# Kernel optimization log

Measured on AMD Instinct MI355X. Metric: run time of the kernel, lower is better.

The kernel has to match this reference:

```python
import jax, jax.numpy as jnp
import numpy as np

B, L, D_MODEL = 2, 4096, 256
D_STATE, D_CONV, EXPAND = 16, 4, 2
D_INNER = EXPAND * D_MODEL
DT_RANK = D_MODEL // 16
D_FF = 2048


def setup_inputs() -> dict:
    key = jax.random.key(0)
    ks = jax.random.split(key, 14)
    s = 0.02
    A_log = jnp.log(jnp.tile(jnp.arange(1, D_STATE + 1, dtype=jnp.float32), (D_INNER, 1)))
    return {
        "x": jax.random.normal(ks[0], (B, L, D_MODEL), jnp.float32),
        "in_proj_w": jax.random.normal(ks[1], (2 * D_INNER, D_MODEL), jnp.float32) * s,
        "conv_w": jax.random.normal(ks[2], (D_INNER, D_CONV), jnp.float32) * s,
        "conv_b": jax.random.normal(ks[3], (D_INNER,), jnp.float32) * s,
        "x_proj_w": jax.random.normal(ks[4], (DT_RANK + 2 * D_STATE, D_INNER), jnp.float32) * s,
        "dt_proj_w": jax.random.normal(ks[5], (D_INNER, DT_RANK), jnp.float32) * s,
        "dt_proj_b": jax.random.uniform(ks[6], (D_INNER,), jnp.float32, -4.0, -2.0),
        "A_log": A_log,
        "D": jnp.ones((D_INNER,), jnp.float32),
        "out_proj_w": jax.random.normal(ks[7], (D_MODEL, D_INNER), jnp.float32) * s,
        "lin1_w": jax.random.normal(ks[8], (D_FF, D_MODEL), jnp.float32) * s,
        "lin1_b": jnp.zeros((D_FF,), jnp.float32),
        "lin2_w": jax.random.normal(ks[9], (D_FF, D_FF), jnp.float32) * s,
        "lin2_b": jnp.zeros((D_FF,), jnp.float32),
    }


def reference(x, in_proj_w, conv_w, conv_b, x_proj_w, dt_proj_w, dt_proj_b,
              A_log, D, out_proj_w, lin1_w, lin1_b, lin2_w, lin2_b):
    b, l, _ = x.shape
    d_inner = conv_w.shape[0]
    d_state = A_log.shape[1]
    dt_rank = dt_proj_w.shape[1]
    d_conv = conv_w.shape[1]

    # in_proj -> split into x and gate z
    xz = x @ in_proj_w.T                       # (B,L,2*Din)
    xin, z = jnp.split(xz, 2, axis=-1)

    # causal depthwise conv1d + SiLU
    xc = jnp.transpose(xin, (0, 2, 1))         # (B,Din,L)
    xc = jax.lax.conv_general_dilated(
        xc, conv_w[:, None, :], (1,), [(d_conv - 1, 0)],
        dimension_numbers=("NCH", "OIH", "NCH"), feature_group_count=d_inner)
    xc = xc + conv_b[None, :, None]
    u = jax.nn.silu(jnp.transpose(xc, (0, 2, 1)))  # (B,L,Din)

    # input-dependent SSM params
    x_dbl = u @ x_proj_w.T                     # (B,L,dt_rank+2*N)
    dt, Bt, Ct = jnp.split(x_dbl, [dt_rank, dt_rank + d_state], axis=-1)
    delta = jax.nn.softplus(dt @ dt_proj_w.T + dt_proj_b)  # (B,L,Din)

    A = -jnp.exp(A_log)                        # (Din,N)
    dA = jnp.exp(delta[..., None] * A)         # (B,L,Din,N)
    dBu = delta[..., None] * Bt[:, :, None, :] * u[..., None]  # (B,L,Din,N)

    def step(h, inp):
        dA_t, dBu_t, C_t = inp
        h = dA_t * h + dBu_t                   # (B,Din,N)
        y = jnp.einsum("bdn,bn->bd", h, C_t)
        return h, y

    h0 = jnp.zeros((b, d_inner, d_state), x.dtype)
    _, ys = jax.lax.scan(step, h0, (jnp.swapaxes(dA, 0, 1),
                                    jnp.swapaxes(dBu, 0, 1),
                                    jnp.swapaxes(Ct, 0, 1)))
    y = jnp.swapaxes(ys, 0, 1) + u * D         # (B,L,Din)
    y = y * jax.nn.silu(z)
    m = y @ out_proj_w.T                       # (B,L,d_model)

    # trailing MLP: lin2(relu(lin1(.)))
    h1 = jax.nn.relu(m @ lin1_w.T + lin1_b)
    return h1 @ lin2_w.T + lin2_b
```

## Files before the change

### kernel.cpp

```cpp
#include <hip/hip_runtime.h>
#include <hip/hip_bf16.h>
#include <stdint.h>

#define BB  2
#define LL  4096
#define DM  256
#define DI  512
#define NST 16
#define DTR 16
#define DFF 2048
#define ML  (BB*LL)

#define NCHUNK 128
#define CHUNK  32
#define BDN    (BB*DI*NST)

typedef __attribute__((ext_vector_type(8))) short s16x8;
typedef __attribute__((ext_vector_type(4))) float f32x4;

__device__ __forceinline__ ushort f2bf(float f) {
  union { float f; uint32_t u; } v; v.f = f;
  return (ushort)((v.u + 0x7FFFu + ((v.u >> 16) & 1u)) >> 16);
}

__device__ __forceinline__ void async16(const void* g, void* l) {
  __builtin_amdgcn_global_load_lds(
      (const __attribute__((address_space(1))) void*)g,
      (__attribute__((address_space(3))) void*)l, 16, 0, 0);
}

__global__ void k_f2b(const float* __restrict__ src, ushort* __restrict__ dst, int n4) {
  int i = blockIdx.x * 256 + threadIdx.x;
  if (i >= n4) return;
  f32x4 v = ((const f32x4*)src)[i];
  *(ushort4*)&dst[i * 4] = make_ushort4(f2bf(v[0]), f2bf(v[1]), f2bf(v[2]), f2bf(v[3]));
}

__global__ void k_xprojw(const float* __restrict__ src, ushort* __restrict__ dst) {
  int i = blockIdx.x * 256 + threadIdx.x;
  if (i >= 128 * DI / 4) return;
  int e = i * 4;
  int r = e >> 9;
  int c = e & 511;
  ushort4 o;
  if (r < DTR + 2 * NST) {
    f32x4 v = *(const f32x4*)&src[r * DI + c];
    o = make_ushort4(f2bf(v[0]), f2bf(v[1]), f2bf(v[2]), f2bf(v[3]));
  } else {
    o = make_ushort4(0, 0, 0, 0);
  }
  *(ushort4*)&dst[e] = o;
}

template<int OUTF, int OUTB, int BIAS, int RELU>
__global__ __launch_bounds__(256)
void k_gemm(const ushort* __restrict__ A, const ushort* __restrict__ W,
            const float* __restrict__ bias,
            float* __restrict__ outF, ushort* __restrict__ outB,
            int M, int N, int K) {
  __shared__ __align__(16) ushort AsB[3][128 * 32];
  __shared__ __align__(16) ushort BsB[3][128 * 32];
  const int tid  = threadIdx.x;
  const int lane = tid & 63;
  const int wv   = tid >> 6;

  const int nwg  = gridDim.x * gridDim.y;
  const int flat = blockIdx.y * gridDim.x + blockIdx.x;
  const int cpx  = nwg >> 3;
  const int swz  = (nwg & 7) ? flat : (flat & 7) * cpx + (flat >> 3);
  const int m0 = (swz / gridDim.x) << 7;
  const int n0 = (swz % gridDim.x) << 7;

  const int wr = (wv >> 1) << 6;
  const int wc = (wv & 1) << 6;
  const int lr = lane & 15;
  const int hi = lane >> 4;

  f32x4 acc[4][4] = {};

  const int sr0 = (wv << 5) + (lane >> 2);
  const int sc  = lane & 3;
  const int nt = K >> 5;

  auto STAGE = [&](int t, int bi) {
    const int k0 = t << 5;
#pragma unroll
    for (int j = 0; j < 2; ++j) {
      const int r  = sr0 + j * 16;
      const int cs = sc ^ ((r >> 1) & 3);
      async16(A + (size_t)(m0 + r) * K + k0 + cs * 8, &AsB[bi][((wv << 5) + j * 16) * 32]);
      async16(W + (size_t)(n0 + r) * K + k0 + cs * 8, &BsB[bi][((wv << 5) + j * 16) * 32]);
    }
  };

  STAGE(0, 0);
  STAGE(1, 1);

  int cur = 0;
  for (int t = 0; t < nt; ++t) {
    if (t + 1 < nt) { asm volatile("s_waitcnt vmcnt(4)" ::: "memory"); }
    else            { asm volatile("s_waitcnt vmcnt(0)" ::: "memory"); }
    __builtin_amdgcn_s_barrier();
    __builtin_amdgcn_sched_barrier(0);

    if (t + 2 < nt) {
      int nx2 = cur + 2; if (nx2 >= 3) nx2 -= 3;
      STAGE(t + 2, nx2);
    }

    const ushort* As = AsB[cur];
    const ushort* Bs = BsB[cur];
    s16x8 af[4], bf_[4];
#pragma unroll
    for (int mi = 0; mi < 4; ++mi) {
      const int row = wr + mi * 16 + lr;
      af[mi] = *(const s16x8*)&As[row * 32 + ((hi ^ ((row >> 1) & 3)) << 3)];
    }
#pragma unroll
    for (int ni = 0; ni < 4; ++ni) {
      const int row = wc + ni * 16 + lr;
      bf_[ni] = *(const s16x8*)&Bs[row * 32 + ((hi ^ ((row >> 1) & 3)) << 3)];
    }
    asm volatile("s_waitcnt lgkmcnt(0)" ::: "memory");
    __builtin_amdgcn_sched_barrier(0);

    __builtin_amdgcn_s_setprio(1);
#pragma unroll
    for (int mi = 0; mi < 4; ++mi)
#pragma unroll
      for (int ni = 0; ni < 4; ++ni)
        acc[mi][ni] = __builtin_amdgcn_mfma_f32_16x16x32_bf16(af[mi], bf_[ni], acc[mi][ni], 0, 0, 0);
    __builtin_amdgcn_s_setprio(0);

    cur = (cur + 1 == 3) ? 0 : cur + 1;
  }

#pragma unroll
  for (int mi = 0; mi < 4; ++mi) {
#pragma unroll
    for (int ni = 0; ni < 4; ++ni) {
      const int gc = n0 + wc + ni * 16 + lr;
      const float b = BIAS ? bias[gc] : 0.f;
#pragma unroll
      for (int i = 0; i < 4; ++i) {
        const int gr = m0 + wr + mi * 16 + (hi << 2) + i;
        float v = acc[mi][ni][i] + b;
        if (RELU) v = fmaxf(v, 0.f);
        if (OUTF) outF[(size_t)gr * N + gc] = v;
        if (OUTB) outB[(size_t)gr * N + gc] = f2bf(v);
      }
    }
  }
}

template<int OUTF, int OUTB, int BIAS, int RELU>
__global__ __launch_bounds__(512, 2)
void k_gemm256(const ushort* __restrict__ A, const ushort* __restrict__ W,
               const float* __restrict__ bias,
               float* __restrict__ outF, ushort* __restrict__ outB,
               int M, int N, int K) {
  __shared__ __align__(16) ushort AsB[4][256 * 32];
  __shared__ __align__(16) ushort BsB[4][256 * 32];
  const int tid  = threadIdx.x;
  const int lane = tid & 63;
  const int wv   = tid >> 6;

  const int nwg  = gridDim.x * gridDim.y;
  const int flat = blockIdx.y * gridDim.x + blockIdx.x;
  const int cpx  = nwg >> 3;
  const int swz  = (nwg & 7) ? flat : (flat & 7) * cpx + (flat >> 3);
  const int m0 = (swz / gridDim.x) << 8;
  const int n0 = (swz % gridDim.x) << 8;

  const int wrM = (wv >> 2) << 7;
  const int wcN = (wv & 3) << 6;
  const int lr = lane & 15;
  const int hi = lane >> 4;

  f32x4 acc[8][4] = {};

  const int sr0 = (wv << 5) + (lane >> 2);
  const int sc  = lane & 3;
  const int nt  = K >> 5;

  auto STAGE = [&](int t, int bi) {
    const int k0 = t << 5;
#pragma unroll
    for (int j = 0; j < 2; ++j) {
      const int r  = sr0 + j * 16;
      const int cs = sc ^ ((r >> 1) & 3);
      async16(A + (size_t)(m0 + r) * K + k0 + cs * 8, &AsB[bi][((wv << 5) + j * 16) * 32]);
      async16(W + (size_t)(n0 + r) * K + k0 + cs * 8, &BsB[bi][((wv << 5) + j * 16) * 32]);
    }
  };

  STAGE(0, 0);
  STAGE(1, 1);
  STAGE(2, 2);

  int cur = 0;
  for (int t = 0; t < nt; ++t) {
    const int fly = nt - 1 - t;
    if (fly >= 2)      { asm volatile("s_waitcnt vmcnt(8)" ::: "memory"); }
    else if (fly == 1) { asm volatile("s_waitcnt vmcnt(4)" ::: "memory"); }
    else               { asm volatile("s_waitcnt vmcnt(0)" ::: "memory"); }
    __builtin_amdgcn_s_barrier();
    __builtin_amdgcn_sched_barrier(0);

    if (t + 3 < nt) STAGE(t + 3, (cur + 3) & 3);

    const ushort* As = AsB[cur];
    const ushort* Bs = BsB[cur];
    s16x8 bf_[4], af[8];
#pragma unroll
    for (int ni = 0; ni < 4; ++ni) {
      const int row = wcN + ni * 16 + lr;
      bf_[ni] = *(const s16x8*)&Bs[row * 32 + ((hi ^ ((row >> 1) & 3)) << 3)];
    }
#pragma unroll
    for (int mi = 0; mi < 8; ++mi) {
      const int row = wrM + mi * 16 + lr;
      af[mi] = *(const s16x8*)&As[row * 32 + ((hi ^ ((row >> 1) & 3)) << 3)];
    }
    asm volatile("s_waitcnt lgkmcnt(0)" ::: "memory");
    __builtin_amdgcn_sched_barrier(0);

    __builtin_amdgcn_s_setprio(1);
#pragma unroll
    for (int mi = 0; mi < 8; ++mi)
#pragma unroll
      for (int ni = 0; ni < 4; ++ni)
        acc[mi][ni] = __builtin_amdgcn_mfma_f32_16x16x32_bf16(af[mi], bf_[ni], acc[mi][ni], 0, 0, 0);
    __builtin_amdgcn_s_setprio(0);

    cur = (cur + 1) & 3;
  }

#pragma unroll
  for (int mi = 0; mi < 8; ++mi) {
#pragma unroll
    for (int ni = 0; ni < 4; ++ni) {
      const int gc = n0 + wcN + ni * 16 + lr;
      const float b = BIAS ? bias[gc] : 0.f;
#pragma unroll
      for (int i = 0; i < 4; ++i) {
        const int gr = m0 + wrM + mi * 16 + (hi << 2) + i;
        float v = acc[mi][ni][i] + b;
        if (RELU) v = fmaxf(v, 0.f);
        if (OUTF) outF[(size_t)gr * N + gc] = v;
        if (OUTB) outB[(size_t)gr * N + gc] = f2bf(v);
      }
    }
  }
}

__global__ void k_conv(const float* __restrict__ xz, const float* __restrict__ cw,
                       const float* __restrict__ cb,
                       float* __restrict__ u, ushort* __restrict__ u_bf) {
  const int i = blockIdx.x * 256 + threadIdx.x;
  if (i >= ML * DI / 4) return;
  const int d4 = i & (DI / 4 - 1);
  const int bl = i / (DI / 4);
  const int l  = bl & (LL - 1);
  const int d  = d4 << 2;
  f32x4 acc;
  acc[0] = cb[d]; acc[1] = cb[d + 1]; acc[2] = cb[d + 2]; acc[3] = cb[d + 3];
#pragma unroll
  for (int j = 0; j < 4; ++j) {
    const int lj = l - 3 + j;
    if (lj >= 0) {
      const f32x4 xv = *(const f32x4*)&xz[(size_t)(bl + j - 3) * 1024 + d];
      acc[0] += xv[0] * cw[(d + 0) * 4 + j];
      acc[1] += xv[1] * cw[(d + 1) * 4 + j];
      acc[2] += xv[2] * cw[(d + 2) * 4 + j];
      acc[3] += xv[3] * cw[(d + 3) * 4 + j];
    }
  }
  f32x4 o;
#pragma unroll
  for (int c = 0; c < 4; ++c) o[c] = acc[c] / (1.f + __expf(-acc[c]));
  *(f32x4*)&u[(size_t)bl * DI + d] = o;
  *(ushort4*)&u_bf[(size_t)bl * DI + d] =
      make_ushort4(f2bf(o[0]), f2bf(o[1]), f2bf(o[2]), f2bf(o[3]));
}

__global__ __launch_bounds__(256)
void k_scan1(const float* __restrict__ u, const float* __restrict__ xdbl,
             const float* __restrict__ A_log, const float* __restrict__ dtw,
             const float* __restrict__ dtb,
             float* __restrict__ Pw, float* __restrict__ Sw) {
  const int c = blockIdx.x;
  const int b = blockIdx.y >> 1;
  const int d = ((blockIdx.y & 1) << 8) + threadIdx.x;
  __shared__ float sdt[CHUNK][16], sB[CHUNK][16];
  {
    const int i = threadIdx.x * 2;
    const int t = i >> 4, n = i & 15;
    const size_t g = ((size_t)b * LL + (size_t)c * CHUNK + t) * 128 + n;
    *(float2*)&sdt[t][n] = *(const float2*)&xdbl[g];
    *(float2*)&sB[t][n]  = *(const float2*)&xdbl[g + DTR];
  }
  float An[16], wreg[16];
#pragma unroll
  for (int j = 0; j < 4; ++j) {
    f32x4 a = *(const f32x4*)&A_log[d * 16 + j * 4];
    f32x4 w = *(const f32x4*)&dtw[d * 16 + j * 4];
#pragma unroll
    for (int q = 0; q < 4; ++q) { An[j * 4 + q] = -__expf(a[q]); wreg[j * 4 + q] = w[q]; }
  }
  const float bd = dtb[d];
  float P[16], S[16];
#pragma unroll
  for (int n = 0; n < 16; ++n) { P[n] = 1.f; S[n] = 0.f; }
  __syncthreads();

  const size_t rowbase = ((size_t)b * LL + (size_t)c * CHUNK) * DI + d;
  float ut = u[rowbase];
  for (int t = 0; t < CHUNK; ++t) {
    const float ut_n = (t + 1 < CHUNK) ? u[rowbase + (size_t)(t + 1) * DI] : 0.f;
    float a = bd;
#pragma unroll
    for (int k2 = 0; k2 < 16; ++k2) a = fmaf(sdt[t][k2], wreg[k2], a);
    const float dt = (a > 15.f) ? a : log1pf(__expf(a));
    const float k = dt * ut;
#pragma unroll
    for (int n = 0; n < 16; ++n) {
      const float dA = __expf(dt * An[n]);
      S[n] = fmaf(dA, S[n], k * sB[t][n]);
      P[n] *= dA;
    }
    ut = ut_n;
  }
  float* Pp = Pw + ((size_t)c * BDN) + ((size_t)b * DI + d) * 16;
  float* Sp = Sw + ((size_t)c * BDN) + ((size_t)b * DI + d) * 16;
#pragma unroll
  for (int j = 0; j < 4; ++j) {
    f32x4 pv, sv;
#pragma unroll
    for (int q = 0; q < 4; ++q) { pv[q] = P[j * 4 + q]; sv[q] = S[j * 4 + q]; }
    *(f32x4*)&Pp[j * 4] = pv;
    *(f32x4*)&Sp[j * 4] = sv;
  }
}

__global__ void k_scan2(float* __restrict__ Pw, const float* __restrict__ Sw) {
  const int f = blockIdx.x * 256 + threadIdx.x;
  float h = 0.f;
#pragma unroll 4
  for (int c = 0; c < NCHUNK; ++c) {
    const float Pc = Pw[(size_t)c * BDN + f];
    const float Sc = Sw[(size_t)c * BDN + f];
    Pw[(size_t)c * BDN + f] = h;
    h = fmaf(Pc, h, Sc);
  }
}

__global__ __launch_bounds__(256)
void k_scan3(const float* __restrict__ u, const float* __restrict__ xdbl,
             const float* __restrict__ xz, const float* __restrict__ A_log,
             const float* __restrict__ dtw, const float* __restrict__ dtb,
             const float* __restrict__ Dp,
             const float* __restrict__ Hs, ushort* __restrict__ y_bf) {
  const int c = blockIdx.x;
  const int b = blockIdx.y >> 1;
  const int d = ((blockIdx.y & 1) << 8) + threadIdx.x;
  __shared__ float sdt[CHUNK][16], sB[CHUNK][16], sC[CHUNK][16];
  {
    const int i = threadIdx.x * 2;
    const int t = i >> 4, n = i & 15;
    const size_t g = ((size_t)b * LL + (size_t)c * CHUNK + t) * 128 + n;
    *(float2*)&sdt[t][n] = *(const float2*)&xdbl[g];
    *(float2*)&sB[t][n]  = *(const float2*)&xdbl[g + DTR];
    *(float2*)&sC[t][n]  = *(const float2*)&xdbl[g + DTR + NST];
  }
  float An[16], wreg[16];
#pragma unroll
  for (int j = 0; j < 4; ++j) {
    f32x4 a = *(const f32x4*)&A_log[d * 16 + j * 4];
    f32x4 w = *(const f32x4*)&dtw[d * 16 + j * 4];
#pragma unroll
    for (int q = 0; q < 4; ++q) { An[j * 4 + q] = -__expf(a[q]); wreg[j * 4 + q] = w[q]; }
  }
  const float bd = dtb[d];
  float h[16];
  {
    const float* Hp = Hs + ((size_t)c * BDN) + ((size_t)b * DI + d) * 16;
#pragma unroll
    for (int j = 0; j < 4; ++j) {
      f32x4 v = *(const f32x4*)&Hp[j * 4];
#pragma unroll
      for (int q = 0; q < 4; ++q) h[j * 4 + q] = v[q];
    }
  }
  const float Dd = Dp[d];
  __syncthreads();

  const size_t rowbase = ((size_t)b * LL + (size_t)c * CHUNK) * DI + d;
  const size_t zbase   = ((size_t)b * LL + (size_t)c * CHUNK) * 1024 + DI + d;
  float ut = u[rowbase];
  float zt = xz[zbase];
  for (int t = 0; t < CHUNK; ++t) {
    float ut_n = 0.f, zt_n = 0.f;
    if (t + 1 < CHUNK) {
      ut_n = u[rowbase + (size_t)(t + 1) * DI];
      zt_n = xz[zbase + (size_t)(t + 1) * 1024];
    }
    float a = bd;
#pragma unroll
    for (int k2 = 0; k2 < 16; ++k2) a = fmaf(sdt[t][k2], wreg[k2], a);
    const float dt = (a > 15.f) ? a : log1pf(__expf(a));
    const float k = dt * ut;
    float y = 0.f;
#pragma unroll
    for (int n = 0; n < 16; ++n) {
      const float dA = __expf(dt * An[n]);
      h[n] = fmaf(dA, h[n], k * sB[t][n]);
      y = fmaf(h[n], sC[t][n], y);
    }
    y = (y + ut * Dd) * (zt / (1.f + __expf(-zt)));
    y_bf[rowbase + (size_t)t * DI] = f2bf(y);
    ut = ut_n; zt = zt_n;
  }
}

extern "C" void kernel_launch(void* const* d_in, const int* in_sizes, int n_in,
                              void* d_out, int out_size, void* d_ws, size_t ws_size,
                              hipStream_t stream) {
  const float* x          = (const float*)d_in[0];
  const float* in_proj_w  = (const float*)d_in[1];
  const float* conv_w     = (const float*)d_in[2];
  const float* conv_b     = (const float*)d_in[3];
  const float* x_proj_w   = (const float*)d_in[4];
  const float* dt_proj_w  = (const float*)d_in[5];
  const float* dt_proj_b  = (const float*)d_in[6];
  const float* A_log      = (const float*)d_in[7];
  const float* Dp         = (const float*)d_in[8];
  const float* out_proj_w = (const float*)d_in[9];
  const float* lin1_w     = (const float*)d_in[10];
  const float* lin1_b     = (const float*)d_in[11];
  const float* lin2_w     = (const float*)d_in[12];
  const float* lin2_b     = (const float*)d_in[13];
  float* out = (float*)d_out;

  char* p = (char*)d_ws;
  auto carve = [&](size_t bytes) -> char* {
    char* r = p;
    p += (bytes + 255) & ~(size_t)255;
    return r;
  };
  ushort* x_bf   = (ushort*)carve((size_t)ML * DM * 2);
  ushort* wip_bf = (ushort*)carve((size_t)2 * DI * DM * 2);
  float*  xz     = (float*) carve((size_t)ML * 1024 * 4);
  float*  u      = (float*) carve((size_t)ML * DI * 4);
  ushort* u_bf   = (ushort*)carve((size_t)ML * DI * 2);
  ushort* xpw_bf = (ushort*)carve((size_t)128 * DI * 2);
  float*  xdbl   = (float*) carve((size_t)ML * 128 * 4);
  ushort* y_bf   = (ushort*)carve((size_t)ML * DI * 2);
  ushort* opw_bf = (ushort*)carve((size_t)DM * DI * 2);
  ushort* l1w_bf = (ushort*)carve((size_t)DFF * DM * 2);
  float*  Pws    = (float*) carve((size_t)NCHUNK * BDN * 4);
  float*  Sws    = (float*) carve((size_t)NCHUNK * BDN * 4);
  ushort* m_bf   = u_bf;
  ushort* h1_bf  = (ushort*)xz;
  ushort* l2w_bf = (ushort*)u;

  k_f2b<<<(ML * DM / 4 + 255) / 256, 256, 0, stream>>>(x, x_bf, ML * DM / 4);
  k_f2b<<<(2 * DI * DM / 4 + 255) / 256, 256, 0, stream>>>(in_proj_w, wip_bf, 2 * DI * DM / 4);
  k_gemm<1, 0, 0, 0><<<dim3(1024 / 128, ML / 128), 256, 0, stream>>>(
      x_bf, wip_bf, nullptr, xz, nullptr, ML, 1024, DM);
  k_conv<<<(ML * DI / 4 + 255) / 256, 256, 0, stream>>>(xz, conv_w, conv_b, u, u_bf);
  k_xprojw<<<(128 * DI / 4 + 255) / 256, 256, 0, stream>>>(x_proj_w, xpw_bf);
  k_gemm<1, 0, 0, 0><<<dim3(1, ML / 128), 256, 0, stream>>>(
      u_bf, xpw_bf, nullptr, xdbl, nullptr, ML, 128, DI);
  k_scan1<<<dim3(NCHUNK, BB * 2), 256, 0, stream>>>(u, xdbl, A_log, dt_proj_w,
                                                    dt_proj_b, Pws, Sws);
  k_scan2<<<BDN / 256, 256, 0, stream>>>(Pws, Sws);
  k_scan3<<<dim3(NCHUNK, BB * 2), 256, 0, stream>>>(u, xdbl, xz, A_log, dt_proj_w,
                                                    dt_proj_b, Dp, Pws, y_bf);
  k_f2b<<<(DM * DI / 4 + 255) / 256, 256, 0, stream>>>(out_proj_w, opw_bf, DM * DI / 4);
  k_gemm<0, 1, 0, 0><<<dim3(DM / 128, ML / 128), 256, 0, stream>>>(
      y_bf, opw_bf, nullptr, nullptr, m_bf, ML, DM, DI);
  k_f2b<<<(DFF * DM / 4 + 255) / 256, 256, 0, stream>>>(lin1_w, l1w_bf, DFF * DM / 4);
  k_gemm256<0, 1, 1, 1><<<dim3(DFF / 256, ML / 256), 512, 0, stream>>>(
      m_bf, l1w_bf, lin1_b, nullptr, h1_bf, ML, DFF, DM);
  k_f2b<<<(DFF * DFF / 4 + 255) / 256, 256, 0, stream>>>(lin2_w, l2w_bf, DFF * DFF / 4);
  k_gemm256<1, 0, 1, 0><<<dim3(DFF / 256, ML / 256), 512, 0, stream>>>(
      h1_bf, l2w_bf, lin2_b, out, nullptr, ML, DFF, DFF);
}
```

Baseline: 369.5 us.

## Double-buffer LDS fragment registers to overlap ds_reads with MFMA in GEMM

```diff
diff --git a/kernel.cpp b/kernel.cpp
--- a/kernel.cpp
+++ b/kernel.cpp
@@ -194,46 +194,68 @@
     }
   };
 
+  auto DSREAD = [&](s16x8 (&af)[8], s16x8 (&bf_)[4], int bi) {
+    const ushort* As = AsB[bi];
+    const ushort* Bs = BsB[bi];
+#pragma unroll
+    for (int ni = 0; ni < 4; ++ni) {
+      const int row = wcN + ni * 16 + lr;
+      bf_[ni] = *(const s16x8*)&Bs[row * 32 + ((hi ^ ((row >> 1) & 3)) << 3)];
+    }
+#pragma unroll
+    for (int mi = 0; mi < 8; ++mi) {
+      const int row = wrM + mi * 16 + lr;
+      af[mi] = *(const s16x8*)&As[row * 32 + ((hi ^ ((row >> 1) & 3)) << 3)];
+    }
+  };
+
+  auto MFMA = [&](s16x8 (&af)[8], s16x8 (&bf_)[4]) {
+    __builtin_amdgcn_s_setprio(1);
+#pragma unroll
+    for (int mi = 0; mi < 8; ++mi)
+#pragma unroll
+      for (int ni = 0; ni < 4; ++ni)
+        acc[mi][ni] = __builtin_amdgcn_mfma_f32_16x16x32_bf16(af[mi], bf_[ni], acc[mi][ni], 0, 0, 0);
+    __builtin_amdgcn_s_setprio(0);
+    __builtin_amdgcn_sched_barrier(0);
+  };
+
+  auto WAITV = [&](int tiles_beyond) {
+    if (tiles_beyond >= 2)      { asm volatile("s_waitcnt vmcnt(8)" ::: "memory"); }
+    else if (tiles_beyond == 1) { asm volatile("s_waitcnt vmcnt(4)" ::: "memory"); }
+    else                        { asm volatile("s_waitcnt vmcnt(0)" ::: "memory"); }
+  };
+
+  s16x8 afE[8], bfE[4];
+  s16x8 afO[8], bfO[4];
+
   STAGE(0, 0);
   STAGE(1, 1);
   STAGE(2, 2);
-
-  int cur = 0;
-  for (int t = 0; t < nt; ++t) {
-    const int fly = nt - 1 - t;
-    if (fly >= 2)      { asm volatile("s_waitcnt vmcnt(8)" ::: "memory"); }
-    else if (fly == 1) { asm volatile("s_waitcnt vmcnt(4)" ::: "memory"); }
-    else               { asm volatile("s_waitcnt vmcnt(0)" ::: "memory"); }
+  WAITV(2);
+  __builtin_amdgcn_s_barrier();
+  DSREAD(afE, bfE, 0);
+  STAGE(3, 3);
+  __builtin_amdgcn_sched_barrier(0);
+
+  for (int s = 0; s < nt; s += 2) {
+    WAITV(nt - 2 - s);
+    asm volatile("s_waitcnt lgkmcnt(0)" ::: "memory");
     __builtin_amdgcn_s_barrier();
     __builtin_amdgcn_sched_barrier(0);
-
-    if (t + 3 < nt) STAGE(t + 3, (cur + 3) & 3);
-
-    const ushort* As = AsB[cur];
-    const ushort* Bs = BsB[cur];
-    s16x8 bf_[4], af[8];
-#pragma unroll
-    for (int ni = 0; ni < 4; ++ni) {
-      const int row = wcN + ni * 16 + lr;
-      bf_[ni] = *(const s16x8*)&Bs[row * 32 + ((hi ^ ((row >> 1) & 3)) << 3)];
-    }
-#pragma unroll
-    for (int mi = 0; mi < 8; ++mi) {
-      const int row = wrM + mi * 16 + lr;
-      af[mi] = *(const s16x8*)&As[row * 32 + ((hi ^ ((row >> 1) & 3)) << 3)];
-    }
+    if (s + 1 < nt) DSREAD(afO, bfO, (s + 1) & 3);
+    if (s + 4 < nt) STAGE(s + 4, (s + 4) & 3);
+    __builtin_amdgcn_sched_barrier(0);
+    MFMA(afE, bfE);
+
+    WAITV(nt - 3 - s);
     asm volatile("s_waitcnt lgkmcnt(0)" ::: "memory");
-    __builtin_amdgcn_sched_barrier(0);
-
-    __builtin_amdgcn_s_setprio(1);
-#pragma unroll
-    for (int mi = 0; mi < 8; ++mi)
-#pragma unroll
-      for (int ni = 0; ni < 4; ++ni)
-        acc[mi][ni] = __builtin_amdgcn_mfma_f32_16x16x32_bf16(af[mi], bf_[ni], acc[mi][ni], 0, 0, 0);
-    __builtin_amdgcn_s_setprio(0);
-
-    cur = (cur + 1) & 3;
+    __builtin_amdgcn_s_barrier();
+    __builtin_amdgcn_sched_barrier(0);
+    if (s + 2 < nt) DSREAD(afE, bfE, (s + 2) & 3);
+    if (s + 5 < nt) STAGE(s + 5, (s + 5) & 3);
+    __builtin_amdgcn_sched_barrier(0);
+    MFMA(afO, bfO);
   }
 
 #pragma unroll
```

Measured after the change: 345.1 us. 1.07x faster.
